# Optimization experiments

Hardware: AMD Instinct MI355X
Metric: run time of the kernel (lower is better)

Reference implementation:

```python
import jax, jax.numpy as jnp
import numpy as np

ALPHA = 0.02
NEG = -9e15

def lrelu(x):
    return jnp.where(x >= 0, x, ALPHA * x)

def layer_norm(x, eps=1e-5):
    m = jnp.mean(x, axis=-1, keepdims=True)
    v = jnp.var(x, axis=-1, keepdims=True)
    return (x - m) * jax.lax.rsqrt(v + eps)

def setup_inputs() -> dict:
    key = jax.random.key(0)
    ks = jax.random.split(key, 10)
    B, N, F_IN, D = 8, 2048, 10, 128
    h = jax.random.normal(ks[0], (B, N, F_IN), jnp.float32)
    adj = jax.random.randint(ks[1], (B, N, N), 0, 2, jnp.int32)
    s = 0.1
    return {
        "h": h,
        "adj": adj,
        "W1": jax.random.normal(ks[2], (D, F_IN), jnp.float32) * s,
        "b1": jax.random.normal(ks[3], (D,), jnp.float32) * s,
        "Wg": jax.random.normal(ks[4], (D, D), jnp.float32) * s,
        "bg": jax.random.normal(ks[5], (D,), jnp.float32) * s,
        "a1": jax.random.normal(ks[6], (D,), jnp.float32) * s,
        "a2": jax.random.normal(ks[7], (D,), jnp.float32) * s,
        "W2": jax.random.normal(ks[8], (2, D), jnp.float32) * s,
        "b2": jax.random.normal(ks[9], (2,), jnp.float32) * s,
    }

def reference(h, adj, W1, b1, Wg, bg, a1, a2, W2, b2):
    # fc1 + layernorm + leakyrelu
    x = h @ W1.T + b1                      # [B,N,128]
    x = lrelu(layer_norm(x))
    # GAT layer
    Wh = x @ Wg.T + bg                     # [B,N,128]
    e1 = Wh @ a1                           # [B,N]
    e2 = Wh @ a2                           # [B,N]
    e = lrelu(e1[:, :, None] + e2[:, None, :])  # [B,N,N]
    e = jnp.where(adj != 0, e, NEG)
    attn = jax.nn.softmax(e, axis=2)
    hp = jnp.einsum('bij,bjd->bid', attn, Wh)    # [B,N,128]
    hp = lrelu(layer_norm(hp))
    # global max pool over nodes
    pooled = jnp.max(hp, axis=1)           # [B,128]
    out = pooled @ W2.T + b2               # [B,2]
    return jax.nn.log_softmax(out, axis=-1)
```

## Files before the change

kernel.cpp:

```cpp
#include <hip/hip_runtime.h>

#define B 8
#define N 2048
#define FIN 10
#define D 128
#define ALPHA 0.02f
#define LOG2E 1.44269504088896340736f
#define BR 32
#define NBLK_ATTN 256

typedef short bf8 __attribute__((ext_vector_type(8)));
typedef short s4v __attribute__((ext_vector_type(4)));
typedef float f32x4 __attribute__((ext_vector_type(4)));
typedef unsigned u4v __attribute__((ext_vector_type(4)));

__device__ __forceinline__ float lrelu(float x) { return x >= 0.f ? x : ALPHA * x; }

__device__ __forceinline__ short f2b(float f) {
    unsigned u = __float_as_uint(f);
    return (short)((u + 0x7fffu + ((u >> 16) & 1u)) >> 16);
}

__device__ __forceinline__ float fexp2(float x) {
#if __has_builtin(__builtin_amdgcn_exp2f)
    return __builtin_amdgcn_exp2f(x);
#else
    return exp2f(x);
#endif
}

__device__ __forceinline__ unsigned pack2(float lo, float hi) {
#if __has_builtin(__builtin_amdgcn_perm)
    return __builtin_amdgcn_perm(__float_as_uint(hi), __float_as_uint(lo), 0x07060302u);
#else
    return (__float_as_uint(hi) & 0xFFFF0000u) | (__float_as_uint(lo) >> 16);
#endif
}

__device__ __forceinline__ unsigned enc_key(float v) {
    unsigned b = __float_as_uint(v);
    return (b & 0x80000000u) ? ~b : (b | 0x80000000u);
}
__device__ __forceinline__ float dec_key(unsigned k) {
    unsigned b = (k & 0x80000000u) ? (k & 0x7fffffffu) : ~k;
    return __uint_as_float(b);
}

__global__ __launch_bounds__(256) void k_prep(
    const float* __restrict__ Wg, unsigned short* __restrict__ Wgb,
    unsigned* __restrict__ pooled, unsigned* __restrict__ cnt)
{
    const int g = blockIdx.x * 256 + threadIdx.x;
    float4 f = *(const float4*)&Wg[g * 4];
    s4v v;
    v[0] = f2b(f.x); v[1] = f2b(f.y); v[2] = f2b(f.z); v[3] = f2b(f.w);
    *(s4v*)&Wgb[g * 4] = v;
    if (g < B * D) pooled[g] = 0u;
    if (g == B * D) *cnt = 0u;
}

__global__ __launch_bounds__(256) void k_proj(
    const float* __restrict__ h, const float* __restrict__ W1, const float* __restrict__ b1,
    const unsigned short* __restrict__ Wgb, const float* __restrict__ bg,
    const float* __restrict__ a1, const float* __restrict__ a2,
    unsigned short* __restrict__ WhT, float* __restrict__ e1g, float* __restrict__ e2g)
{
    __shared__ __align__(16) short xep_lds[32 * 136];
    __shared__ __align__(16) short wg_lds[D * 136];
    __shared__ float W1_lds[D * 11];
    __shared__ float h_lds[BR * FIN];
    __shared__ float ep1[2][BR], ep2[2][BR];

    const int t = threadIdx.x;
    const int r0 = blockIdx.x * BR;
    const int bb = r0 >> 11;
    const int jloc = r0 & (N - 1);

    for (int idx = t; idx < D * FIN; idx += 256)
        W1_lds[(idx / FIN) * 11 + (idx % FIN)] = W1[idx];
    for (int idx = t; idx < BR * FIN; idx += 256)
        h_lds[idx] = h[(size_t)r0 * FIN + idx];
    __syncthreads();

    {
        const int dr = t >> 4;
        const int j8 = t & 15;
        #pragma unroll
        for (int pass = 0; pass < 8; pass++) {
            int dd = pass * 16 + dr;
            *(bf8*)&wg_lds[dd * 136 + j8 * 8] = *(const bf8*)&Wgb[dd * D + j8 * 8];
        }
    }

    const int w = t >> 6, lane = t & 63;
    {
        float b1v0 = b1[lane], b1v1 = b1[lane + 64];
        float sA[8], sB[8], smv[8], sqv[8];
        #pragma unroll
        for (int i = 0; i < 8; i++) {
            const float* hr = &h_lds[(w * 8 + i) * FIN];
            float s0 = b1v0, s1 = b1v1;
            #pragma unroll
            for (int k = 0; k < FIN; k++) {
                float hv = hr[k];
                s0 += hv * W1_lds[lane * 11 + k];
                s1 += hv * W1_lds[(lane + 64) * 11 + k];
            }
            sA[i] = s0; sB[i] = s1;
            smv[i] = s0 + s1; sqv[i] = s0 * s0 + s1 * s1;
        }
        #pragma unroll
        for (int m = 1; m <= 32; m <<= 1) {
            #pragma unroll
            for (int i = 0; i < 8; i++) { smv[i] += __shfl_xor(smv[i], m); sqv[i] += __shfl_xor(sqv[i], m); }
        }
        #pragma unroll
        for (int i = 0; i < 8; i++) {
            int r = w * 8 + i;
            float mean = smv[i] * (1.f / D);
            float var  = sqv[i] * (1.f / D) - mean * mean;
            float rs = rsqrtf(var + 1e-5f);
            xep_lds[r * 136 + lane]      = f2b(lrelu((sA[i] - mean) * rs));
            xep_lds[r * 136 + lane + 64] = f2b(lrelu((sB[i] - mean) * rs));
        }
    }
    __syncthreads();

    const int l15 = lane & 15, q = lane >> 4;
    const int mw = w & 1, np = w >> 1;
    f32x4 acc[4];
    #pragma unroll
    for (int nt = 0; nt < 4; nt++)
        #pragma unroll
        for (int r = 0; r < 4; r++) acc[nt][r] = 0.f;

    #pragma unroll
    for (int ks = 0; ks < 4; ks++) {
        bf8 av = *(const bf8*)&xep_lds[(mw * 16 + l15) * 136 + ks * 32 + q * 8];
        #pragma unroll
        for (int nt = 0; nt < 4; nt++) {
            bf8 bv = *(const bf8*)&wg_lds[((np * 4 + nt) * 16 + l15) * 136 + ks * 32 + q * 8];
            acc[nt] = __builtin_amdgcn_mfma_f32_16x16x32_bf16(av, bv, acc[nt], 0, 0, 0);
        }
    }

    float e1p[4] = {0.f, 0.f, 0.f, 0.f}, e2p[4] = {0.f, 0.f, 0.f, 0.f};
    #pragma unroll
    for (int nt = 0; nt < 4; nt++) {
        int col = (np * 4 + nt) * 16 + l15;
        float bgv = bg[col], a1v = a1[col], a2v = a2[col];
        #pragma unroll
        for (int r = 0; r < 4; r++) {
            float v = acc[nt][r] + bgv;
            acc[nt][r] = v;
            e1p[r] += v * a1v;
            e2p[r] += v * a2v;
        }
    }
    #pragma unroll
    for (int m = 1; m <= 8; m <<= 1) {
        #pragma unroll
        for (int r = 0; r < 4; r++) { e1p[r] += __shfl_xor(e1p[r], m); e2p[r] += __shfl_xor(e2p[r], m); }
    }
    if (l15 == 0) {
        #pragma unroll
        for (int r = 0; r < 4; r++) {
            ep1[np][mw * 16 + q * 4 + r] = e1p[r];
            ep2[np][mw * 16 + q * 4 + r] = e2p[r];
        }
    }
    __syncthreads();
    if (t < BR) {
        e1g[r0 + t] = (ep1[0][t] + ep1[1][t]) * LOG2E;
        e2g[r0 + t] = (ep2[0][t] + ep2[1][t]) * LOG2E;
    }
    #pragma unroll
    for (int nt = 0; nt < 4; nt++) {
        int col = (np * 4 + nt) * 16 + l15;
        #pragma unroll
        for (int r = 0; r < 4; r++)
            xep_lds[col * 36 + mw * 16 + q * 4 + r] = f2b(acc[nt][r]);
    }
    __syncthreads();
    {
        const int col = t >> 1, jh = (t & 1) * 16;
        unsigned short* dst = WhT + ((size_t)(bb * D + col)) * N + jloc + jh;
        #pragma unroll
        for (int i2 = 0; i2 < 4; i2++)
            *(uint2*)(dst + i2 * 4) = *(const uint2*)&xep_lds[col * 36 + jh + i2 * 4];
    }
}

struct Stage {
    int4 a0, a1;
    float4 e20, e21;
    bf8 wv[8];
};

__device__ __forceinline__ void load_stage(Stage& s, const int* adjp,
        const float* e2p, const unsigned short* whp, int c) {
    const int off = c * 32;
    s.a0  = *(const int4*)(adjp + off);
    s.a1  = *(const int4*)(adjp + off + 4);
    s.e20 = *(const float4*)(e2p + off);
    s.e21 = *(const float4*)(e2p + off + 4);
    #pragma unroll
    for (int nt = 0; nt < 8; nt++)
        s.wv[nt] = *(const bf8*)(whp + (size_t)nt * 16 * N + off);
}

__device__ __forceinline__ void consume(const Stage& s, float e1v,
        f32x4* acc, f32x4& accl, bf8 ones) {
    float t0 = e1v + s.e20.x, t1 = e1v + s.e20.y, t2 = e1v + s.e20.z, t3 = e1v + s.e20.w;
    float t4 = e1v + s.e21.x, t5 = e1v + s.e21.y, t6 = e1v + s.e21.z, t7 = e1v + s.e21.w;
    float p0 = s.a0.x ? fexp2(fmaxf(t0, ALPHA * t0)) : 0.f;
    float p1 = s.a0.y ? fexp2(fmaxf(t1, ALPHA * t1)) : 0.f;
    float p2 = s.a0.z ? fexp2(fmaxf(t2, ALPHA * t2)) : 0.f;
    float p3 = s.a0.w ? fexp2(fmaxf(t3, ALPHA * t3)) : 0.f;
    float p4 = s.a1.x ? fexp2(fmaxf(t4, ALPHA * t4)) : 0.f;
    float p5 = s.a1.y ? fexp2(fmaxf(t5, ALPHA * t5)) : 0.f;
    float p6 = s.a1.z ? fexp2(fmaxf(t6, ALPHA * t6)) : 0.f;
    float p7 = s.a1.w ? fexp2(fmaxf(t7, ALPHA * t7)) : 0.f;
    u4v uu;
    uu.x = pack2(p0, p1); uu.y = pack2(p2, p3);
    uu.z = pack2(p4, p5); uu.w = pack2(p6, p7);
    bf8 av = *(bf8*)&uu;
    #pragma unroll
    for (int nt = 0; nt < 8; nt++)
        acc[nt] = __builtin_amdgcn_mfma_f32_16x16x32_bf16(av, s.wv[nt], acc[nt], 0, 0, 0);
    accl = __builtin_amdgcn_mfma_f32_16x16x32_bf16(av, ones, accl, 0, 0, 0);
}

__global__ __launch_bounds__(256) void k_attn(
    const int* __restrict__ adj, const unsigned short* __restrict__ WhT,
    const float* __restrict__ e1g, const float* __restrict__ e2g,
    unsigned* __restrict__ pooled, unsigned* __restrict__ cnt,
    const float* __restrict__ W2, const float* __restrict__ b2,
    float* __restrict__ out)
{
    __shared__ unsigned maxb[4][D];
    __shared__ int finalflag;

    const int t = threadIdx.x;
    const int w = t >> 6, lane = t & 63;
    const int l15 = lane & 15, q = lane >> 4;
    const int bid = blockIdx.x;
    const int b = bid >> 5;
    const int tile = (bid & 31) * 4 + w;
    const int i0 = tile * 16;

    const float e1v = e1g[b * N + i0 + l15];

    const int* adjp = adj + ((size_t)b * N + i0 + l15) * N + q * 8;
    const float* e2p = e2g + b * N + q * 8;
    const unsigned short* whp = WhT + (size_t)b * D * N + (size_t)l15 * N + q * 8;

    f32x4 acc[8], accl;
    #pragma unroll
    for (int nt = 0; nt < 8; nt++)
        #pragma unroll
        for (int r = 0; r < 4; r++) acc[nt][r] = 0.f;
    #pragma unroll
    for (int r = 0; r < 4; r++) accl[r] = 0.f;

    bf8 ones;
    #pragma unroll
    for (int i = 0; i < 8; i++) ones[i] = (short)0x3F80;

    Stage SA, SB;
    load_stage(SA, adjp, e2p, whp, 0);
    load_stage(SB, adjp, e2p, whp, 1);

    for (int c = 0; c < N / 32; c += 2) {
        consume(SA, e1v, acc, accl, ones);
        if (c + 2 < N / 32) load_stage(SA, adjp, e2p, whp, c + 2);
        consume(SB, e1v, acc, accl, ones);
        if (c + 3 < N / 32) load_stage(SB, adjp, e2p, whp, c + 3);
    }

    float smr[4], sqr[4];
    #pragma unroll
    for (int r = 0; r < 4; r++) {
        float rinv = 1.f / accl[r];
        float sm = 0.f, sq = 0.f;
        #pragma unroll
        for (int nt = 0; nt < 8; nt++) {
            float v = acc[nt][r] * rinv;
            acc[nt][r] = v;
            sm += v; sq += v * v;
        }
        smr[r] = sm; sqr[r] = sq;
    }
    #pragma unroll
    for (int m = 1; m <= 8; m <<= 1) {
        #pragma unroll
        for (int r = 0; r < 4; r++) { smr[r] += __shfl_xor(smr[r], m); sqr[r] += __shfl_xor(sqr[r], m); }
    }
    float mx[8];
    #pragma unroll
    for (int nt = 0; nt < 8; nt++) mx[nt] = -1e30f;
    #pragma unroll
    for (int r = 0; r < 4; r++) {
        float mean = smr[r] * (1.f / D);
        float var  = sqr[r] * (1.f / D) - mean * mean;
        float rs = rsqrtf(var + 1e-5f);
        #pragma unroll
        for (int nt = 0; nt < 8; nt++) {
            float v = lrelu((acc[nt][r] - mean) * rs);
            mx[nt] = fmaxf(mx[nt], v);
        }
    }
    #pragma unroll
    for (int m = 16; m <= 32; m <<= 1) {
        #pragma unroll
        for (int nt = 0; nt < 8; nt++) mx[nt] = fmaxf(mx[nt], __shfl_xor(mx[nt], m));
    }
    if (lane < 16) {
        #pragma unroll
        for (int nt = 0; nt < 8; nt++) maxb[w][nt * 16 + lane] = enc_key(mx[nt]);
    }
    __syncthreads();
    if (t < D) {
        unsigned m01 = maxb[0][t] > maxb[1][t] ? maxb[0][t] : maxb[1][t];
        unsigned m23 = maxb[2][t] > maxb[3][t] ? maxb[2][t] : maxb[3][t];
        atomicMax(&pooled[b * D + t], m01 > m23 ? m01 : m23);
    }
    __syncthreads();

    if (t == 0) {
        __threadfence();
        unsigned old = atomicAdd(cnt, 1u);
        finalflag = (old == NBLK_ATTN - 1) ? 1 : 0;
    }
    __syncthreads();
    if (finalflag) {
        const int fb = t >> 5;
        const int fq = t & 31;
        float s0 = 0.f, s1 = 0.f;
        #pragma unroll
        for (int m = 0; m < 4; m++) {
            int dd = fq + 32 * m;
            unsigned key = __hip_atomic_load(&pooled[fb * D + dd], __ATOMIC_RELAXED,
                                             __HIP_MEMORY_SCOPE_AGENT);
            float v = dec_key(key);
            s0 += v * W2[dd];
            s1 += v * W2[D + dd];
        }
        #pragma unroll
        for (int m = 1; m <= 16; m <<= 1) { s0 += __shfl_xor(s0, m); s1 += __shfl_xor(s1, m); }
        if (fq == 0) {
            float o0 = s0 + b2[0], o1 = s1 + b2[1];
            float mxv = fmaxf(o0, o1);
            float ls = logf(__expf(o0 - mxv) + __expf(o1 - mxv));
            out[fb * 2 + 0] = o0 - mxv - ls;
            out[fb * 2 + 1] = o1 - mxv - ls;
        }
    }
}

extern "C" void kernel_launch(void* const* d_in, const int* in_sizes, int n_in,
                              void* d_out, int out_size, void* d_ws, size_t ws_size,
                              hipStream_t stream) {
    const float* h   = (const float*)d_in[0];
    const int*   adj = (const int*)d_in[1];
    const float* W1  = (const float*)d_in[2];
    const float* b1  = (const float*)d_in[3];
    const float* Wg  = (const float*)d_in[4];
    const float* bg  = (const float*)d_in[5];
    const float* a1  = (const float*)d_in[6];
    const float* a2  = (const float*)d_in[7];
    const float* W2  = (const float*)d_in[8];
    const float* b2  = (const float*)d_in[9];
    float* out = (float*)d_out;

    unsigned short* WhT = (unsigned short*)d_ws;
    float* e1g = (float*)((char*)d_ws + (size_t)B * D * N * 2);
    float* e2g = e1g + (size_t)B * N;
    unsigned* pooled = (unsigned*)(e2g + (size_t)B * N);
    unsigned* cnt = pooled + (size_t)B * D;
    unsigned short* Wgb = (unsigned short*)(cnt + 4);

    k_prep<<<16, 256, 0, stream>>>(Wg, Wgb, pooled, cnt);
    k_proj<<<(B * N) / BR, 256, 0, stream>>>(h, W1, b1, Wgb, bg, a1, a2,
                                             WhT, e1g, e2g);
    k_attn<<<NBLK_ATTN, 256, 0, stream>>>(adj, WhT, e1g, e2g, pooled, cnt,
                                          W2, b2, out);
}
```

Baseline: 274.8 us.

## Split attention row tile across waves by feature half and key half

Each block now handles one 16-row tile. Its four waves split the work two ways: across two halves of the 128 output features and across two halves of the 2048 keys. Partial outputs and row sums are combined through shared memory before the layernorm and the max-pool. This raises the grid from 256 to 1024 blocks for better occupancy on the many CUs and halves the per-wave accumulator and register footprint. The cost is that each wave recomputes the exp scores for its key half twice (once per feature half), adjacency is read twice, and an extra LDS reduction and barrier are added.

```diff
diff --git a/kernel.cpp b/kernel.cpp
--- a/kernel.cpp
+++ b/kernel.cpp
@@ -7,7 +7,7 @@
 #define ALPHA 0.02f
 #define LOG2E 1.44269504088896340736f
 #define BR 32
-#define NBLK_ATTN 256
+#define NBLK_ATTN 1024
 
 typedef short bf8 __attribute__((ext_vector_type(8)));
 typedef short s4v __attribute__((ext_vector_type(4)));
@@ -194,7 +194,7 @@
 struct Stage {
     int4 a0, a1;
     float4 e20, e21;
-    bf8 wv[8];
+    bf8 wv[4];
 };
 
 __device__ __forceinline__ void load_stage(Stage& s, const int* adjp,
@@ -205,7 +205,7 @@
     s.e20 = *(const float4*)(e2p + off);
     s.e21 = *(const float4*)(e2p + off + 4);
     #pragma unroll
-    for (int nt = 0; nt < 8; nt++)
+    for (int nt = 0; nt < 4; nt++)
         s.wv[nt] = *(const bf8*)(whp + (size_t)nt * 16 * N + off);
 }
 
@@ -226,7 +226,7 @@
     uu.z = pack2(p4, p5); uu.w = pack2(p6, p7);
     bf8 av = *(bf8*)&uu;
     #pragma unroll
-    for (int nt = 0; nt < 8; nt++)
+    for (int nt = 0; nt < 4; nt++)
         acc[nt] = __builtin_amdgcn_mfma_f32_16x16x32_bf16(av, s.wv[nt], acc[nt], 0, 0, 0);
     accl = __builtin_amdgcn_mfma_f32_16x16x32_bf16(av, ones, accl, 0, 0, 0);
 }
@@ -238,26 +238,28 @@
     const float* __restrict__ W2, const float* __restrict__ b2,
     float* __restrict__ out)
 {
-    __shared__ unsigned maxb[4][D];
+    __shared__ float ored[2][16][132];
+    __shared__ float lred[2][16];
     __shared__ int finalflag;
 
     const int t = threadIdx.x;
     const int w = t >> 6, lane = t & 63;
     const int l15 = lane & 15, q = lane >> 4;
-    const int bid = blockIdx.x;
-    const int b = bid >> 5;
-    const int tile = (bid & 31) * 4 + w;
-    const int i0 = tile * 16;
+    const int ds = w >> 1;
+    const int js = w & 1;
+    const int b = blockIdx.y;
+    const int i0 = blockIdx.x * 16;
 
     const float e1v = e1g[b * N + i0 + l15];
 
-    const int* adjp = adj + ((size_t)b * N + i0 + l15) * N + q * 8;
-    const float* e2p = e2g + b * N + q * 8;
-    const unsigned short* whp = WhT + (size_t)b * D * N + (size_t)l15 * N + q * 8;
-
-    f32x4 acc[8], accl;
-    #pragma unroll
-    for (int nt = 0; nt < 8; nt++)
+    const int jb = js * (N / 2);
+    const int* adjp = adj + ((size_t)b * N + i0 + l15) * N + jb + q * 8;
+    const float* e2p = e2g + b * N + jb + q * 8;
+    const unsigned short* whp = WhT + ((size_t)b * D + ds * 64 + l15) * N + jb + q * 8;
+
+    f32x4 acc[4], accl;
+    #pragma unroll
+    for (int nt = 0; nt < 4; nt++)
         #pragma unroll
         for (int r = 0; r < 4; r++) acc[nt][r] = 0.f;
     #pragma unroll
@@ -271,59 +273,53 @@
     load_stage(SA, adjp, e2p, whp, 0);
     load_stage(SB, adjp, e2p, whp, 1);
 
-    for (int c = 0; c < N / 32; c += 2) {
+    for (int c = 0; c < 32; c += 2) {
         consume(SA, e1v, acc, accl, ones);
-        if (c + 2 < N / 32) load_stage(SA, adjp, e2p, whp, c + 2);
+        if (c + 2 < 32) load_stage(SA, adjp, e2p, whp, c + 2);
         consume(SB, e1v, acc, accl, ones);
-        if (c + 3 < N / 32) load_stage(SB, adjp, e2p, whp, c + 3);
-    }
-
-    float smr[4], sqr[4];
-    #pragma unroll
-    for (int r = 0; r < 4; r++) {
-        float rinv = 1.f / accl[r];
-        float sm = 0.f, sq = 0.f;
-        #pragma unroll
-        for (int nt = 0; nt < 8; nt++) {
-            float v = acc[nt][r] * rinv;
-            acc[nt][r] = v;
-            sm += v; sq += v * v;
-        }
-        smr[r] = sm; sqr[r] = sq;
-    }
-    #pragma unroll
-    for (int m = 1; m <= 8; m <<= 1) {
-        #pragma unroll
-        for (int r = 0; r < 4; r++) { smr[r] += __shfl_xor(smr[r], m); sqr[r] += __shfl_xor(sqr[r], m); }
-    }
-    float mx[8];
-    #pragma unroll
-    for (int nt = 0; nt < 8; nt++) mx[nt] = -1e30f;
-    #pragma unroll
-    for (int r = 0; r < 4; r++) {
-        float mean = smr[r] * (1.f / D);
-        float var  = sqr[r] * (1.f / D) - mean * mean;
+        if (c + 3 < 32) load_stage(SB, adjp, e2p, whp, c + 3);
+    }
+
+    #pragma unroll
+    for (int nt = 0; nt < 4; nt++) {
+        int col = ds * 64 + nt * 16 + l15;
+        #pragma unroll
+        for (int r = 0; r < 4; r++)
+            ored[js][q * 4 + r][col] = acc[nt][r];
+    }
+    if (ds == 0 && l15 == 0) {
+        #pragma unroll
+        for (int r = 0; r < 4; r++) lred[js][q * 4 + r] = accl[r];
+    }
+    __syncthreads();
+
+    const int rr = t >> 4, cg = (t & 15) * 8;
+    float v[8];
+    float linv = 1.f / (lred[0][rr] + lred[1][rr]);
+    float sm = 0.f, sq = 0.f;
+    #pragma unroll
+    for (int k = 0; k < 8; k++) {
+        float o = (ored[0][rr][cg + k] + ored[1][rr][cg + k]) * linv;
+        v[k] = o;
+        sm += o; sq += o * o;
+    }
+    #pragma unroll
+    for (int m = 1; m <= 8; m <<= 1) { sm += __shfl_xor(sm, m); sq += __shfl_xor(sq, m); }
+    {
+        float mean = sm * (1.f / D);
+        float var  = sq * (1.f / D) - mean * mean;
         float rs = rsqrtf(var + 1e-5f);
         #pragma unroll
-        for (int nt = 0; nt < 8; nt++) {
-            float v = lrelu((acc[nt][r] - mean) * rs);
-            mx[nt] = fmaxf(mx[nt], v);
-        }
-    }
-    #pragma unroll
-    for (int m = 16; m <= 32; m <<= 1) {
-        #pragma unroll
-        for (int nt = 0; nt < 8; nt++) mx[nt] = fmaxf(mx[nt], __shfl_xor(mx[nt], m));
-    }
-    if (lane < 16) {
-        #pragma unroll
-        for (int nt = 0; nt < 8; nt++) maxb[w][nt * 16 + lane] = enc_key(mx[nt]);
-    }
-    __syncthreads();
+        for (int k = 0; k < 8; k++)
+            ored[0][rr][cg + k] = lrelu((v[k] - mean) * rs);
+    }
+    __syncthreads();
+
     if (t < D) {
-        unsigned m01 = maxb[0][t] > maxb[1][t] ? maxb[0][t] : maxb[1][t];
-        unsigned m23 = maxb[2][t] > maxb[3][t] ? maxb[2][t] : maxb[3][t];
-        atomicMax(&pooled[b * D + t], m01 > m23 ? m01 : m23);
+        float mxv = ored[0][0][t];
+        #pragma unroll
+        for (int r = 1; r < 16; r++) mxv = fmaxf(mxv, ored[0][r][t]);
+        atomicMax(&pooled[b * D + t], enc_key(mxv));
     }
     __syncthreads();
 
@@ -342,9 +338,9 @@
             int dd = fq + 32 * m;
             unsigned key = __hip_atomic_load(&pooled[fb * D + dd], __ATOMIC_RELAXED,
                                              __HIP_MEMORY_SCOPE_AGENT);
-            float v = dec_key(key);
-            s0 += v * W2[dd];
-            s1 += v * W2[D + dd];
+            float vv = dec_key(key);
+            s0 += vv * W2[dd];
+            s1 += vv * W2[D + dd];
         }
         #pragma unroll
         for (int m = 1; m <= 16; m <<= 1) { s0 += __shfl_xor(s0, m); s1 += __shfl_xor(s1, m); }
@@ -383,6 +379,6 @@
     k_prep<<<16, 256, 0, stream>>>(Wg, Wgb, pooled, cnt);
     k_proj<<<(B * N) / BR, 256, 0, stream>>>(h, W1, b1, Wgb, bg, a1, a2,
                                              WhT, e1g, e2g);
-    k_attn<<<NBLK_ATTN, 256, 0, stream>>>(adj, WhT, e1g, e2g, pooled, cnt,
-                                          W2, b2, out);
-}
+    k_attn<<<dim3(N / 16, B), 256, 0, stream>>>(adj, WhT, e1g, e2g, pooled, cnt,
+                                                W2, b2, out);
+}
```

After: 335.4 us. +22.0%, slower.

## Pack adjacency into bitmask in a pre-pass and re-split attention tiles

Applied to the files above, without the earlier changes.

A new pre-pass kernel reads the int32 adjacency matrix once and packs it into a per-row bitmask using wave ballots. The attention kernel then reads the compact mask instead of the full int32 rows. The attention kernel is also restructured: each block handles 32 rows, with waves split across row halves and two 64-column halves of D, which needs a shared-memory exchange for the layernorm statistics. It now launches 512 blocks with a 2-blocks-per-CU launch bound. The full adjacency read still happens, now in the pack kernel, which adds a serial kernel, a bitmask written to and read back from memory, and more WhT traffic across column-split waves.

```diff
diff --git a/kernel.cpp b/kernel.cpp
--- a/kernel.cpp
+++ b/kernel.cpp
@@ -7,7 +7,7 @@
 #define ALPHA 0.02f
 #define LOG2E 1.44269504088896340736f
 #define BR 32
-#define NBLK_ATTN 256
+#define NBLK_ATTN ((N / 32) * B)
 
 typedef short bf8 __attribute__((ext_vector_type(8)));
 typedef short s4v __attribute__((ext_vector_type(4)));
@@ -46,17 +46,37 @@
     return __uint_as_float(b);
 }
 
-__global__ __launch_bounds__(256) void k_prep(
+__global__ __launch_bounds__(256) void k_pack(
+    const int* __restrict__ adj, unsigned* __restrict__ bm,
     const float* __restrict__ Wg, unsigned short* __restrict__ Wgb,
     unsigned* __restrict__ pooled, unsigned* __restrict__ cnt)
 {
-    const int g = blockIdx.x * 256 + threadIdx.x;
-    float4 f = *(const float4*)&Wg[g * 4];
-    s4v v;
-    v[0] = f2b(f.x); v[1] = f2b(f.y); v[2] = f2b(f.z); v[3] = f2b(f.w);
-    *(s4v*)&Wgb[g * 4] = v;
-    if (g < B * D) pooled[g] = 0u;
-    if (g == B * D) *cnt = 0u;
+    const int t = threadIdx.x;
+    const int gid = blockIdx.x * 256 + t;
+    if (gid < 4096) {
+        float4 f = *(const float4*)&Wg[gid * 4];
+        s4v v;
+        v[0] = f2b(f.x); v[1] = f2b(f.y); v[2] = f2b(f.z); v[3] = f2b(f.w);
+        *(s4v*)&Wgb[gid * 4] = v;
+    }
+    if (gid < B * D) pooled[gid] = 0u;
+    if (gid == B * D) *cnt = 0u;
+
+    const int w = t >> 6, lane = t & 63;
+    const int wg = blockIdx.x * 4 + w;
+    for (int rr = 0; rr < 16; rr++) {
+        const int row = wg * 16 + rr;
+        const int* ap = adj + (size_t)row * N + lane;
+        unsigned myw = 0;
+        #pragma unroll
+        for (int it = 0; it < 32; it++) {
+            int a = ap[it * 64];
+            unsigned long long m = __ballot(a != 0);
+            myw = (lane == 2 * it)     ? (unsigned)m         : myw;
+            myw = (lane == 2 * it + 1) ? (unsigned)(m >> 32) : myw;
+        }
+        bm[(size_t)row * (N / 32) + lane] = myw;
+    }
 }
 
 __global__ __launch_bounds__(256) void k_proj(
@@ -191,73 +211,33 @@
     }
 }
 
-struct Stage {
-    int4 a0, a1;
-    float4 e20, e21;
-    bf8 wv[8];
-};
-
-__device__ __forceinline__ void load_stage(Stage& s, const int* adjp,
-        const float* e2p, const unsigned short* whp, int c) {
-    const int off = c * 32;
-    s.a0  = *(const int4*)(adjp + off);
-    s.a1  = *(const int4*)(adjp + off + 4);
-    s.e20 = *(const float4*)(e2p + off);
-    s.e21 = *(const float4*)(e2p + off + 4);
-    #pragma unroll
-    for (int nt = 0; nt < 8; nt++)
-        s.wv[nt] = *(const bf8*)(whp + (size_t)nt * 16 * N + off);
-}
-
-__device__ __forceinline__ void consume(const Stage& s, float e1v,
-        f32x4* acc, f32x4& accl, bf8 ones) {
-    float t0 = e1v + s.e20.x, t1 = e1v + s.e20.y, t2 = e1v + s.e20.z, t3 = e1v + s.e20.w;
-    float t4 = e1v + s.e21.x, t5 = e1v + s.e21.y, t6 = e1v + s.e21.z, t7 = e1v + s.e21.w;
-    float p0 = s.a0.x ? fexp2(fmaxf(t0, ALPHA * t0)) : 0.f;
-    float p1 = s.a0.y ? fexp2(fmaxf(t1, ALPHA * t1)) : 0.f;
-    float p2 = s.a0.z ? fexp2(fmaxf(t2, ALPHA * t2)) : 0.f;
-    float p3 = s.a0.w ? fexp2(fmaxf(t3, ALPHA * t3)) : 0.f;
-    float p4 = s.a1.x ? fexp2(fmaxf(t4, ALPHA * t4)) : 0.f;
-    float p5 = s.a1.y ? fexp2(fmaxf(t5, ALPHA * t5)) : 0.f;
-    float p6 = s.a1.z ? fexp2(fmaxf(t6, ALPHA * t6)) : 0.f;
-    float p7 = s.a1.w ? fexp2(fmaxf(t7, ALPHA * t7)) : 0.f;
-    u4v uu;
-    uu.x = pack2(p0, p1); uu.y = pack2(p2, p3);
-    uu.z = pack2(p4, p5); uu.w = pack2(p6, p7);
-    bf8 av = *(bf8*)&uu;
-    #pragma unroll
-    for (int nt = 0; nt < 8; nt++)
-        acc[nt] = __builtin_amdgcn_mfma_f32_16x16x32_bf16(av, s.wv[nt], acc[nt], 0, 0, 0);
-    accl = __builtin_amdgcn_mfma_f32_16x16x32_bf16(av, ones, accl, 0, 0, 0);
-}
-
-__global__ __launch_bounds__(256) void k_attn(
-    const int* __restrict__ adj, const unsigned short* __restrict__ WhT,
+__global__ __launch_bounds__(256, 2) void k_attn(
+    const unsigned* __restrict__ bm, const unsigned short* __restrict__ WhT,
     const float* __restrict__ e1g, const float* __restrict__ e2g,
     unsigned* __restrict__ pooled, unsigned* __restrict__ cnt,
     const float* __restrict__ W2, const float* __restrict__ b2,
     float* __restrict__ out)
 {
-    __shared__ unsigned maxb[4][D];
+    __shared__ float statsp[2][32][2];
+    __shared__ unsigned maxb[2][D];
     __shared__ int finalflag;
 
     const int t = threadIdx.x;
+    const int b = blockIdx.y;
+    const int i0 = blockIdx.x * 32;
     const int w = t >> 6, lane = t & 63;
     const int l15 = lane & 15, q = lane >> 4;
-    const int bid = blockIdx.x;
-    const int b = bid >> 5;
-    const int tile = (bid & 31) * 4 + w;
-    const int i0 = tile * 16;
-
-    const float e1v = e1g[b * N + i0 + l15];
-
-    const int* adjp = adj + ((size_t)b * N + i0 + l15) * N + q * 8;
-    const float* e2p = e2g + b * N + q * 8;
-    const unsigned short* whp = WhT + (size_t)b * D * N + (size_t)l15 * N + q * 8;
-
-    f32x4 acc[8], accl;
-    #pragma unroll
-    for (int nt = 0; nt < 8; nt++)
+    const int mw = w & 1, np = w >> 1;
+
+    const int rowg = i0 + mw * 16 + l15;
+    const float e1v = e1g[b * N + rowg];
+    const unsigned* maskp = bm + (size_t)(b * N + rowg) * (N / 32);
+    const float4* e2p4 = (const float4*)(e2g + (size_t)b * N);
+    const unsigned short* whp = WhT + (size_t)(b * D + np * 64 + l15) * N;
+
+    f32x4 acc[4], accl;
+    #pragma unroll
+    for (int nt = 0; nt < 4; nt++)
         #pragma unroll
         for (int r = 0; r < 4; r++) acc[nt][r] = 0.f;
     #pragma unroll
@@ -267,25 +247,50 @@
     #pragma unroll
     for (int i = 0; i < 8; i++) ones[i] = (short)0x3F80;
 
-    Stage SA, SB;
-    load_stage(SA, adjp, e2p, whp, 0);
-    load_stage(SB, adjp, e2p, whp, 1);
-
-    for (int c = 0; c < N / 32; c += 2) {
-        consume(SA, e1v, acc, accl, ones);
-        if (c + 2 < N / 32) load_stage(SA, adjp, e2p, whp, c + 2);
-        consume(SB, e1v, acc, accl, ones);
-        if (c + 3 < N / 32) load_stage(SB, adjp, e2p, whp, c + 3);
+    for (int c4 = 0; c4 < N / 128; c4++) {
+        int4 m4 = *(const int4*)(maskp + c4 * 4);
+        unsigned mws[4] = {(unsigned)m4.x, (unsigned)m4.y, (unsigned)m4.z, (unsigned)m4.w};
+        #pragma unroll
+        for (int cc = 0; cc < 4; cc++) {
+            const int c = c4 * 4 + cc;
+            const unsigned mbyte = (mws[cc] >> (q * 8)) & 0xFFu;
+            float4 ea = e2p4[c * 8 + q * 2];
+            float4 eb = e2p4[c * 8 + q * 2 + 1];
+            bf8 bv0 = *(const bf8*)(whp + (size_t)(0 * 16) * N + c * 32 + q * 8);
+            bf8 bv1 = *(const bf8*)(whp + (size_t)(1 * 16) * N + c * 32 + q * 8);
+            bf8 bv2 = *(const bf8*)(whp + (size_t)(2 * 16) * N + c * 32 + q * 8);
+            bf8 bv3 = *(const bf8*)(whp + (size_t)(3 * 16) * N + c * 32 + q * 8);
+
+            float ev[8] = {ea.x, ea.y, ea.z, ea.w, eb.x, eb.y, eb.z, eb.w};
+            float pv[8];
+            #pragma unroll
+            for (int jj = 0; jj < 8; jj++) {
+                float tt = e1v + ev[jj];
+                float sel = (mbyte & (1u << jj)) ? tt : -1e30f;
+                float lr = fmaxf(sel, ALPHA * sel);
+                pv[jj] = fexp2(lr);
+            }
+            u4v uu;
+            uu.x = pack2(pv[0], pv[1]); uu.y = pack2(pv[2], pv[3]);
+            uu.z = pack2(pv[4], pv[5]); uu.w = pack2(pv[6], pv[7]);
+            bf8 av = *(bf8*)&uu;
+
+            acc[0] = __builtin_amdgcn_mfma_f32_16x16x32_bf16(av, bv0, acc[0], 0, 0, 0);
+            acc[1] = __builtin_amdgcn_mfma_f32_16x16x32_bf16(av, bv1, acc[1], 0, 0, 0);
+            acc[2] = __builtin_amdgcn_mfma_f32_16x16x32_bf16(av, bv2, acc[2], 0, 0, 0);
+            acc[3] = __builtin_amdgcn_mfma_f32_16x16x32_bf16(av, bv3, acc[3], 0, 0, 0);
+            accl   = __builtin_amdgcn_mfma_f32_16x16x32_bf16(av, ones, accl, 0, 0, 0);
+        }
     }
 
     float smr[4], sqr[4];
     #pragma unroll
     for (int r = 0; r < 4; r++) {
-        float rinv = 1.f / accl[r];
+        float linv = 1.f / accl[r];
         float sm = 0.f, sq = 0.f;
         #pragma unroll
-        for (int nt = 0; nt < 8; nt++) {
-            float v = acc[nt][r] * rinv;
+        for (int nt = 0; nt < 4; nt++) {
+            float v = acc[nt][r] * linv;
             acc[nt][r] = v;
             sm += v; sq += v * v;
         }
@@ -296,16 +301,26 @@
         #pragma unroll
         for (int r = 0; r < 4; r++) { smr[r] += __shfl_xor(smr[r], m); sqr[r] += __shfl_xor(sqr[r], m); }
     }
-    float mx[8];
-    #pragma unroll
-    for (int nt = 0; nt < 8; nt++) mx[nt] = -1e30f;
+    if (l15 == 0) {
+        #pragma unroll
+        for (int r = 0; r < 4; r++) {
+            statsp[np][mw * 16 + q * 4 + r][0] = smr[r];
+            statsp[np][mw * 16 + q * 4 + r][1] = sqr[r];
+        }
+    }
+    __syncthreads();
+
+    float mx[4] = {-1e30f, -1e30f, -1e30f, -1e30f};
     #pragma unroll
     for (int r = 0; r < 4; r++) {
-        float mean = smr[r] * (1.f / D);
-        float var  = sqr[r] * (1.f / D) - mean * mean;
+        int row = mw * 16 + q * 4 + r;
+        float s0 = statsp[0][row][0] + statsp[1][row][0];
+        float s1 = statsp[0][row][1] + statsp[1][row][1];
+        float mean = s0 * (1.f / D);
+        float var  = s1 * (1.f / D) - mean * mean;
         float rs = rsqrtf(var + 1e-5f);
         #pragma unroll
-        for (int nt = 0; nt < 8; nt++) {
+        for (int nt = 0; nt < 4; nt++) {
             float v = lrelu((acc[nt][r] - mean) * rs);
             mx[nt] = fmaxf(mx[nt], v);
         }
@@ -313,17 +328,17 @@
     #pragma unroll
     for (int m = 16; m <= 32; m <<= 1) {
         #pragma unroll
-        for (int nt = 0; nt < 8; nt++) mx[nt] = fmaxf(mx[nt], __shfl_xor(mx[nt], m));
-    }
-    if (lane < 16) {
-        #pragma unroll
-        for (int nt = 0; nt < 8; nt++) maxb[w][nt * 16 + lane] = enc_key(mx[nt]);
+        for (int nt = 0; nt < 4; nt++) mx[nt] = fmaxf(mx[nt], __shfl_xor(mx[nt], m));
+    }
+    if (q == 0) {
+        #pragma unroll
+        for (int nt = 0; nt < 4; nt++)
+            maxb[mw][np * 64 + nt * 16 + l15] = enc_key(mx[nt]);
     }
     __syncthreads();
     if (t < D) {
-        unsigned m01 = maxb[0][t] > maxb[1][t] ? maxb[0][t] : maxb[1][t];
-        unsigned m23 = maxb[2][t] > maxb[3][t] ? maxb[2][t] : maxb[3][t];
-        atomicMax(&pooled[b * D + t], m01 > m23 ? m01 : m23);
+        unsigned k0 = maxb[0][t], k1 = maxb[1][t];
+        atomicMax(&pooled[b * D + t], k0 > k1 ? k0 : k1);
     }
     __syncthreads();
 
@@ -373,16 +388,19 @@
     const float* b2  = (const float*)d_in[9];
     float* out = (float*)d_out;
 
-    unsigned short* WhT = (unsigned short*)d_ws;
-    float* e1g = (float*)((char*)d_ws + (size_t)B * D * N * 2);
-    float* e2g = e1g + (size_t)B * N;
-    unsigned* pooled = (unsigned*)(e2g + (size_t)B * N);
-    unsigned* cnt = pooled + (size_t)B * D;
-    unsigned short* Wgb = (unsigned short*)(cnt + 4);
-
-    k_prep<<<16, 256, 0, stream>>>(Wg, Wgb, pooled, cnt);
+    char* ws = (char*)d_ws;
+    unsigned short* WhT = (unsigned short*)ws;
+    ws += (size_t)B * D * N * 2;
+    float* e1g = (float*)ws;  ws += (size_t)B * N * 4;
+    float* e2g = (float*)ws;  ws += (size_t)B * N * 4;
+    unsigned* pooled = (unsigned*)ws;  ws += (size_t)B * D * 4;
+    unsigned* cnt = (unsigned*)ws;     ws += 16;
+    unsigned short* Wgb = (unsigned short*)ws;  ws += (size_t)D * D * 2;
+    unsigned* bmask = (unsigned*)ws;
+
+    k_pack<<<256, 256, 0, stream>>>(adj, bmask, Wg, Wgb, pooled, cnt);
     k_proj<<<(B * N) / BR, 256, 0, stream>>>(h, W1, b1, Wgb, bg, a1, a2,
                                              WhT, e1g, e2g);
-    k_attn<<<NBLK_ATTN, 256, 0, stream>>>(adj, WhT, e1g, e2g, pooled, cnt,
-                                          W2, b2, out);
-}
+    k_attn<<<dim3(N / 32, B), 256, 0, stream>>>(bmask, WhT, e1g, e2g, pooled, cnt,
+                                                W2, b2, out);
+}
```

After: 299.5 us. +9.0%, slower.
